# Optimization experiments

Hardware: AMD Instinct MI355X
Metric: run time of the kernel (lower is better)

## Reference

```python
import jax, jax.numpy as jnp
import numpy as np

N = 100000       # nodes
E = 1600000      # edges (avg degree 16)
IN_DIM = 64
HID_DIM = 128
OUT_DIM = 64

def setup_inputs() -> dict:
    key = jax.random.key(0)
    k = jax.random.split(key, 8)
    inp = jax.random.normal(k[0], (IN_DIM, N), dtype=jnp.float32)
    src = jax.random.randint(k[1], (E,), 0, N, dtype=jnp.int32)
    dst = jax.random.randint(k[2], (E,), 0, N, dtype=jnp.int32)
    # Linear params (torch nn.Linear: y = x @ W.T + b)
    s1 = 1.0 / np.sqrt(IN_DIM)
    W1 = jax.random.uniform(k[3], (HID_DIM, IN_DIM), jnp.float32, -s1, s1)
    b1 = jax.random.uniform(k[4], (HID_DIM,), jnp.float32, -s1, s1)
    s2 = 1.0 / np.sqrt(HID_DIM)
    W2 = jax.random.uniform(k[5], (OUT_DIM, HID_DIM), jnp.float32, -s2, s2)
    b2 = jax.random.uniform(k[6], (OUT_DIM,), jnp.float32, -s2, s2)
    return {"inp": inp, "src": src, "dst": dst, "W1": W1, "b1": b1, "W2": W2, "b2": b2}

def reference(inp, src, dst, W1, b1, W2, b2):
    # inp: [in_dim, N] (module passes transposed features)
    X = inp.T                                   # [N, in_dim] node features
    # update_all(copy_src, sum): gather src features, scatter-add at dst
    agg = jax.ops.segment_sum(X[src], dst, num_segments=X.shape[0])  # [N, in_dim]
    h = jax.nn.relu(agg @ W1.T + b1)            # [N, hidden]
    out = h @ W2.T + b2                         # [N, out_dim]
    return out.T                                 # [out_dim, N] (final .t())
```

## Files before the change

kernel.cpp:

```cpp
#include <hip/hip_runtime.h>
#include <hip/hip_bf16.h>
#include <stdint.h>

typedef unsigned short ushort_t;
using short8   = __attribute__((ext_vector_type(8))) short;
using float4v  = __attribute__((ext_vector_type(4))) float;

#define BSH    6
#define BUCKW  64
#define CAP    1536
#define NBMAX  2048
#define TPITCH 266
#define BINB   128

__device__ __forceinline__ float bf2f(ushort_t u) {
    union { unsigned int i; float f; } v;
    v.i = ((unsigned int)u) << 16;
    return v.f;
}
__device__ __forceinline__ ushort_t f2b(float f) {
    union { float f; unsigned int i; } v;
    v.f = f;
    unsigned int u = v.i;
    unsigned int r = (u + 0x7fffu + ((u >> 16) & 1u)) >> 16;
    return (ushort_t)r;
}
__device__ __forceinline__ float blo2f(unsigned v) {
    union { unsigned i; float f; } u; u.i = v << 16; return u.f;
}
__device__ __forceinline__ float bhi2f(unsigned v) {
    union { unsigned i; float f; } u; u.i = v & 0xFFFF0000u; return u.f;
}

__global__ __launch_bounds__(1024) void prep_k(
        const float* __restrict__ inp, ushort_t* __restrict__ X, int N,
        const float* __restrict__ W1, const float* __restrict__ W2,
        ushort_t* __restrict__ w1b, ushort_t* __restrict__ w2b,
        const int* __restrict__ src, const int* __restrict__ dst,
        int* __restrict__ gcur, unsigned* __restrict__ bin, int E,
        int NB, int TB) {
    __shared__ __align__(16) char smem[64 * TPITCH * 2];
    int tid = threadIdx.x;

    if ((int)blockIdx.x < TB) {
        if (blockIdx.x == 0) {
            for (int i = tid; i < 8192; i += 1024) {
                w1b[i] = f2b(W1[i]);
                w2b[i] = f2b(W2[i]);
            }
        }
        ushort_t* tile = (ushort_t*)smem;
        int w    = tid >> 6;
        int lane = tid & 63;
        int n0   = blockIdx.x * 256;
        int col  = (w >> 2) * 64 + lane;
        int nc   = n0 + col;
#pragma unroll
        for (int r = 0; r < 16; ++r) {
            int d = (w & 3) * 16 + r;
            if (nc < N) tile[d * TPITCH + col] = f2b(inp[(size_t)d * N + nc]);
        }
        __syncthreads();
#pragma unroll
        for (int r = 0; r < 16; ++r) {
            int nl = w * 16 + r;
            int n  = n0 + nl;
            if (n < N) X[(size_t)n * 64 + lane] = tile[lane * TPITCH + nl];
        }
    } else {
        int* lcnt  = (int*)smem;
        int* gbase = lcnt + NBMAX;
        int* lcur  = gbase + NBMAX;
        int bid   = blockIdx.x - TB;
        int chunk = (E + BINB - 1) / BINB;
        int s0 = bid * chunk;
        int s1 = s0 + chunk;
        if (s1 > E) s1 = E;

        for (int b = tid; b < NB; b += 1024) lcnt[b] = 0;
        __syncthreads();

        for (int e = s0 + tid; e < s1; e += 1024)
            atomicAdd(&lcnt[dst[e] >> BSH], 1);
        __syncthreads();

        for (int b = tid; b < NB; b += 1024) {
            int c = lcnt[b];
            gbase[b] = c ? atomicAdd(&gcur[b], c) : 0;
            lcur[b]  = 0;
        }
        __syncthreads();

        for (int e = s0 + tid; e < s1; e += 1024) {
            int d = dst[e];
            int b = d >> BSH;
            int pos = gbase[b] + atomicAdd(&lcur[b], 1);
            if (pos < CAP)
                bin[(size_t)b * CAP + pos] =
                    ((unsigned)(d & (BUCKW - 1)) << 24) | (unsigned)src[e];
        }
    }
}

__global__ __launch_bounds__(256) void bagg_k(
        const unsigned* __restrict__ Xu, const unsigned* __restrict__ bin,
        const int* __restrict__ gcur, unsigned* __restrict__ aggu, int N) {
    __shared__ unsigned sl[CAP];
    __shared__ int ecnt[BUCKW];
    __shared__ int sc[BUCKW];
    __shared__ int ecur[BUCKW];
    int tid = threadIdx.x;
    int b   = blockIdx.x;
    int lo  = b << BSH;

    int cnt = gcur[b];
    if (cnt > CAP) cnt = CAP;
    const unsigned* bb = bin + (size_t)b * CAP;

    if (tid < BUCKW) ecnt[tid] = 0;
    __syncthreads();

    for (int i = tid; i < cnt; i += 256)
        atomicAdd(&ecnt[bb[i] >> 24], 1);
    __syncthreads();

    if (tid < BUCKW) sc[tid] = ecnt[tid];
    __syncthreads();
#pragma unroll
    for (int off = 1; off < BUCKW; off <<= 1) {
        int v = 0;
        if (tid < BUCKW && tid >= off) v = sc[tid - off];
        __syncthreads();
        if (tid < BUCKW) sc[tid] += v;
        __syncthreads();
    }
    if (tid < BUCKW) { sc[tid] -= ecnt[tid]; ecur[tid] = 0; }
    __syncthreads();

    for (int i = tid; i < cnt; i += 256) {
        unsigned p = bb[i];
        int nl  = (int)(p >> 24);
        int pos = sc[nl] + atomicAdd(&ecur[nl], 1);
        sl[pos] = p;
    }
    __syncthreads();

    int wave = tid >> 6;
    int lane = tid & 63;
    int half = lane >> 5;
    int c2   = lane & 31;

    for (int n = wave; n < BUCKW; n += 4) {
        int node = lo + n;
        if (node >= N) break;
        int s0 = sc[n];
        int c  = ecnt[n];
        float alo0 = 0.f, ahi0 = 0.f, alo1 = 0.f, ahi1 = 0.f;
        int i = 0;
        for (; i + 16 <= c; i += 16) {
            unsigned p0 = sl[s0 + i +  0 + half], p1 = sl[s0 + i +  2 + half];
            unsigned p2 = sl[s0 + i +  4 + half], p3 = sl[s0 + i +  6 + half];
            unsigned p4 = sl[s0 + i +  8 + half], p5 = sl[s0 + i + 10 + half];
            unsigned p6 = sl[s0 + i + 12 + half], p7 = sl[s0 + i + 14 + half];
            unsigned v0 = Xu[(size_t)(p0 & 0xFFFFFFu) * 32 + c2];
            unsigned v1 = Xu[(size_t)(p1 & 0xFFFFFFu) * 32 + c2];
            unsigned v2 = Xu[(size_t)(p2 & 0xFFFFFFu) * 32 + c2];
            unsigned v3 = Xu[(size_t)(p3 & 0xFFFFFFu) * 32 + c2];
            unsigned v4 = Xu[(size_t)(p4 & 0xFFFFFFu) * 32 + c2];
            unsigned v5 = Xu[(size_t)(p5 & 0xFFFFFFu) * 32 + c2];
            unsigned v6 = Xu[(size_t)(p6 & 0xFFFFFFu) * 32 + c2];
            unsigned v7 = Xu[(size_t)(p7 & 0xFFFFFFu) * 32 + c2];
            alo0 += blo2f(v0); ahi0 += bhi2f(v0);
            alo1 += blo2f(v1); ahi1 += bhi2f(v1);
            alo0 += blo2f(v2); ahi0 += bhi2f(v2);
            alo1 += blo2f(v3); ahi1 += bhi2f(v3);
            alo0 += blo2f(v4); ahi0 += bhi2f(v4);
            alo1 += blo2f(v5); ahi1 += bhi2f(v5);
            alo0 += blo2f(v6); ahi0 += bhi2f(v6);
            alo1 += blo2f(v7); ahi1 += bhi2f(v7);
        }
        for (; i + 2 <= c; i += 2) {
            unsigned p = sl[s0 + i + half];
            unsigned v = Xu[(size_t)(p & 0xFFFFFFu) * 32 + c2];
            alo0 += blo2f(v); ahi0 += bhi2f(v);
        }
        if (i + half < c) {
            unsigned p = sl[s0 + i + half];
            unsigned v = Xu[(size_t)(p & 0xFFFFFFu) * 32 + c2];
            alo1 += blo2f(v); ahi1 += bhi2f(v);
        }
        float alo = alo0 + alo1;
        float ahi = ahi0 + ahi1;
        float blo = __shfl(alo, lane + 32);
        float bhi = __shfl(ahi, lane + 32);
        if (half == 0) {
            alo += blo; ahi += bhi;
            aggu[(size_t)node * 32 + c2] =
                (unsigned)f2b(alo) | ((unsigned)f2b(ahi) << 16);
        }
    }
}

#define HPITCH 136

__global__ __launch_bounds__(256) void mlp_k(
        const ushort_t* __restrict__ aggb,
        const ushort_t* __restrict__ W1, const float* __restrict__ b1,
        const ushort_t* __restrict__ W2, const float* __restrict__ b2,
        float* __restrict__ out, int N) {
    __shared__ ushort_t h_s[4][16 * HPITCH];

    int wave = threadIdx.x >> 6;
    int lane = threadIdx.x & 63;
    int row  = lane & 15;
    int quad = lane >> 4;
    int n0   = blockIdx.x * 64 + wave * 16;

    int anode = n0 + row;
    if (anode > N - 1) anode = N - 1;
    const ushort_t* ap = aggb + (size_t)anode * 64;
    short8 a0 = *(const short8*)(ap + quad * 8);
    short8 a1 = *(const short8*)(ap + 32 + quad * 8);

    float4v zero = {0.f, 0.f, 0.f, 0.f};
    float4v acc[8];
#pragma unroll
    for (int nt = 0; nt < 8; ++nt) acc[nt] = zero;

#pragma unroll
    for (int nt = 0; nt < 8; ++nt) {
        const ushort_t* wp = W1 + (size_t)(nt * 16 + row) * 64 + quad * 8;
        short8 bf0 = *(const short8*)(wp);
        short8 bf1 = *(const short8*)(wp + 32);
        acc[nt] = __builtin_amdgcn_mfma_f32_16x16x32_bf16(a0, bf0, acc[nt], 0, 0, 0);
        acc[nt] = __builtin_amdgcn_mfma_f32_16x16x32_bf16(a1, bf1, acc[nt], 0, 0, 0);
    }

    ushort_t* hw = h_s[wave];
#pragma unroll
    for (int nt = 0; nt < 8; ++nt) {
        float bias = b1[nt * 16 + row];
#pragma unroll
        for (int r = 0; r < 4; ++r) {
            float v = acc[nt][r] + bias;
            v = v > 0.f ? v : 0.f;
            hw[(quad * 4 + r) * HPITCH + nt * 16 + row] = f2b(v);
        }
    }
    __syncthreads();

    short8 a2[4];
#pragma unroll
    for (int kt = 0; kt < 4; ++kt)
        a2[kt] = *(const short8*)(hw + row * HPITCH + kt * 32 + quad * 8);

    float4v acc2[4];
#pragma unroll
    for (int nt = 0; nt < 4; ++nt) acc2[nt] = zero;

#pragma unroll
    for (int nt = 0; nt < 4; ++nt) {
#pragma unroll
        for (int kt = 0; kt < 4; ++kt) {
            short8 bfr = *(const short8*)(W2 + (size_t)(nt * 16 + row) * 128 +
                                          kt * 32 + quad * 8);
            acc2[nt] = __builtin_amdgcn_mfma_f32_16x16x32_bf16(a2[kt], bfr, acc2[nt], 0, 0, 0);
        }
    }

    int node = n0 + quad * 4;
    if (node < N) {
#pragma unroll
        for (int nt = 0; nt < 4; ++nt) {
            int ko = nt * 16 + row;
            float bias = b2[ko];
            float4v pk;
#pragma unroll
            for (int r = 0; r < 4; ++r) pk[r] = acc2[nt][r] + bias;
            *(float4v*)(out + (size_t)ko * N + node) = pk;
        }
    }
}

extern "C" void kernel_launch(void* const* d_in, const int* in_sizes, int n_in,
                              void* d_out, int out_size, void* d_ws, size_t ws_size,
                              hipStream_t stream) {
    const float* inp = (const float*)d_in[0];
    const int*   src = (const int*)d_in[1];
    const int*   dst = (const int*)d_in[2];
    const float* W1  = (const float*)d_in[3];
    const float* b1  = (const float*)d_in[4];
    const float* W2  = (const float*)d_in[5];
    const float* b2  = (const float*)d_in[6];
    float* out = (float*)d_out;

    int N  = in_sizes[0] / 64;
    int E  = in_sizes[1];
    int NB = (N + BUCKW - 1) >> BSH;

    ushort_t* aggb = (ushort_t*)d_ws;
    ushort_t* w1b  = aggb + (size_t)N * 64;
    ushort_t* w2b  = w1b + 8192;
    int*      gcur = (int*)(w2b + 8192);

    char*     ob  = (char*)d_out;
    ushort_t* X   = (ushort_t*)ob;
    unsigned* bin = (unsigned*)(ob + (size_t)N * 64 * 2);

    hipMemsetAsync(gcur, 0, NB * sizeof(int), stream);

    int TB = (N + 255) / 256;
    prep_k<<<TB + BINB, 1024, 0, stream>>>(inp, X, N, W1, W2, w1b, w2b,
                                           src, dst, gcur, bin, E, NB, TB);

    bagg_k<<<NB, 256, 0, stream>>>((const unsigned*)X, bin, gcur,
                                   (unsigned*)aggb, N);

    int tb = (N + 63) / 64;
    mlp_k<<<tb, 256, 0, stream>>>(aggb, w1b, b1, w2b, b2, out, N);
}
```

Before: 204.2 us.

## Replace LDS transpose with register-packed vector stores and batch binning loads

The transpose part of prep_k drops the shared-memory tile. Each thread now reads 16 strided floats for one node, packs them into bf16 pairs and writes two 16-byte vector stores straight to X. The binning part doubles the number of blocks, halves the block size to 512, and unrolls the dst/src loads by 8 so more memory requests are in flight before the LDS atomics. The cost is more global atomics on gcur and more registers per thread, and the column reads from inp are now 128 nodes wide instead of 256.

New measurement: 203.2 us. About the same (-0.5%).

```diff
diff --git a/kernel.cpp b/kernel.cpp
--- a/kernel.cpp
+++ b/kernel.cpp
@@ -5,13 +5,13 @@
 typedef unsigned short ushort_t;
 using short8   = __attribute__((ext_vector_type(8))) short;
 using float4v  = __attribute__((ext_vector_type(4))) float;
+using uint4v   = __attribute__((ext_vector_type(4))) unsigned;
 
 #define BSH    6
 #define BUCKW  64
 #define CAP    1536
 #define NBMAX  2048
-#define TPITCH 266
-#define BINB   128
+#define BINB   256
 
 __device__ __forceinline__ float bf2f(ushort_t u) {
     union { unsigned int i; float f; } v;
@@ -32,72 +32,97 @@
     union { unsigned i; float f; } u; u.i = v & 0xFFFF0000u; return u.f;
 }
 
-__global__ __launch_bounds__(1024) void prep_k(
+__global__ __launch_bounds__(512) void prep_k(
         const float* __restrict__ inp, ushort_t* __restrict__ X, int N,
         const float* __restrict__ W1, const float* __restrict__ W2,
         ushort_t* __restrict__ w1b, ushort_t* __restrict__ w2b,
         const int* __restrict__ src, const int* __restrict__ dst,
         int* __restrict__ gcur, unsigned* __restrict__ bin, int E,
         int NB, int TB) {
-    __shared__ __align__(16) char smem[64 * TPITCH * 2];
+    __shared__ int lcnt[NBMAX];
+    __shared__ int gbase[NBMAX];
+    __shared__ int lcur[NBMAX];
     int tid = threadIdx.x;
 
     if ((int)blockIdx.x < TB) {
         if (blockIdx.x == 0) {
-            for (int i = tid; i < 8192; i += 1024) {
+            for (int i = tid; i < 8192; i += 512) {
                 w1b[i] = f2b(W1[i]);
                 w2b[i] = f2b(W2[i]);
             }
         }
-        ushort_t* tile = (ushort_t*)smem;
-        int w    = tid >> 6;
-        int lane = tid & 63;
-        int n0   = blockIdx.x * 256;
-        int col  = (w >> 2) * 64 + lane;
-        int nc   = n0 + col;
-#pragma unroll
-        for (int r = 0; r < 16; ++r) {
-            int d = (w & 3) * 16 + r;
-            if (nc < N) tile[d * TPITCH + col] = f2b(inp[(size_t)d * N + nc]);
-        }
-        __syncthreads();
-#pragma unroll
-        for (int r = 0; r < 16; ++r) {
-            int nl = w * 16 + r;
-            int n  = n0 + nl;
-            if (n < N) X[(size_t)n * 64 + lane] = tile[lane * TPITCH + nl];
+        int db = tid >> 7;
+        int nl = tid & 127;
+        int nc = blockIdx.x * 128 + nl;
+        if (nc < N) {
+            const float* ip = inp + (size_t)(db * 16) * N + nc;
+            float v[16];
+#pragma unroll
+            for (int r = 0; r < 16; ++r)
+                v[r] = ip[(size_t)r * N];
+            unsigned dw[8];
+#pragma unroll
+            for (int j = 0; j < 8; ++j)
+                dw[j] = (unsigned)f2b(v[2 * j]) | ((unsigned)f2b(v[2 * j + 1]) << 16);
+            unsigned* xp = (unsigned*)X + (size_t)nc * 32 + db * 8;
+            uint4v a = {dw[0], dw[1], dw[2], dw[3]};
+            uint4v b = {dw[4], dw[5], dw[6], dw[7]};
+            *(uint4v*)(xp)     = a;
+            *(uint4v*)(xp + 4) = b;
         }
     } else {
-        int* lcnt  = (int*)smem;
-        int* gbase = lcnt + NBMAX;
-        int* lcur  = gbase + NBMAX;
         int bid   = blockIdx.x - TB;
         int chunk = (E + BINB - 1) / BINB;
         int s0 = bid * chunk;
         int s1 = s0 + chunk;
         if (s1 > E) s1 = E;
 
-        for (int b = tid; b < NB; b += 1024) lcnt[b] = 0;
-        __syncthreads();
-
-        for (int e = s0 + tid; e < s1; e += 1024)
+        for (int b = tid; b < NB; b += 512) lcnt[b] = 0;
+        __syncthreads();
+
+        int e = s0 + tid;
+        for (; e + 512 * 7 < s1; e += 512 * 8) {
+            int d[8];
+#pragma unroll
+            for (int k = 0; k < 8; ++k) d[k] = dst[e + 512 * k];
+#pragma unroll
+            for (int k = 0; k < 8; ++k) atomicAdd(&lcnt[d[k] >> BSH], 1);
+        }
+        for (; e < s1; e += 512)
             atomicAdd(&lcnt[dst[e] >> BSH], 1);
         __syncthreads();
 
-        for (int b = tid; b < NB; b += 1024) {
+        for (int b = tid; b < NB; b += 512) {
             int c = lcnt[b];
             gbase[b] = c ? atomicAdd(&gcur[b], c) : 0;
             lcur[b]  = 0;
         }
         __syncthreads();
 
-        for (int e = s0 + tid; e < s1; e += 1024) {
-            int d = dst[e];
-            int b = d >> BSH;
+        e = s0 + tid;
+        for (; e + 512 * 7 < s1; e += 512 * 8) {
+            int d[8], s[8];
+#pragma unroll
+            for (int k = 0; k < 8; ++k) {
+                d[k] = dst[e + 512 * k];
+                s[k] = src[e + 512 * k];
+            }
+#pragma unroll
+            for (int k = 0; k < 8; ++k) {
+                int b   = d[k] >> BSH;
+                int pos = gbase[b] + atomicAdd(&lcur[b], 1);
+                if (pos < CAP)
+                    bin[(size_t)b * CAP + pos] =
+                        ((unsigned)(d[k] & (BUCKW - 1)) << 24) | (unsigned)s[k];
+            }
+        }
+        for (; e < s1; e += 512) {
+            int dv = dst[e];
+            int b  = dv >> BSH;
             int pos = gbase[b] + atomicAdd(&lcur[b], 1);
             if (pos < CAP)
                 bin[(size_t)b * CAP + pos] =
-                    ((unsigned)(d & (BUCKW - 1)) << 24) | (unsigned)src[e];
+                    ((unsigned)(dv & (BUCKW - 1)) << 24) | (unsigned)src[e];
         }
     }
 }
@@ -309,9 +334,9 @@
 
     hipMemsetAsync(gcur, 0, NB * sizeof(int), stream);
 
-    int TB = (N + 255) / 256;
-    prep_k<<<TB + BINB, 1024, 0, stream>>>(inp, X, N, W1, W2, w1b, w2b,
-                                           src, dst, gcur, bin, E, NB, TB);
+    int TB = (N + 127) / 128;
+    prep_k<<<TB + BINB, 512, 0, stream>>>(inp, X, N, W1, W2, w1b, w2b,
+                                          src, dst, gcur, bin, E, NB, TB);
 
     bagg_k<<<NB, 256, 0, stream>>>((const unsigned*)X, bin, gcur,
                                    (unsigned*)aggb, N);
```
